# Kernel optimization log

Hardware: AMD Instinct MI355X
Metric: run time of the kernel (lower is better)

The kernel has to match this reference:

```python
import jax, jax.numpy as jnp
import numpy as np

B, C, H, W = 4, 3, 1024, 1024
RADII = (8, 16, 32, 64)
EPS = 1e-5  # BatchNorm2d default eps


def _box_sum(x, r, s):
    # depthwise all-ones conv (kernel r, stride s, VALID padding) == summed box
    return jax.lax.reduce_window(x, 0.0, jax.lax.add, (1, 1, r, r), (1, 1, s, s), 'VALID')


def _axis_interp_ac(x, n_out, axis):
    # bilinear (align_corners=True) interpolation along one axis
    n_in = x.shape[axis]
    pos = jnp.arange(n_out, dtype=x.dtype) * ((n_in - 1) / max(n_out - 1, 1))
    i0 = jnp.clip(jnp.floor(pos).astype(jnp.int32), 0, n_in - 2)
    w = pos - i0.astype(x.dtype)
    a = jnp.take(x, i0, axis=axis)
    b = jnp.take(x, i0 + 1, axis=axis)
    shape = [1] * x.ndim
    shape[axis] = n_out
    w = w.reshape(shape)
    return a * (1 - w) + b * w


def _resize_ac(x, oh, ow):
    x = _axis_interp_ac(x, oh, 2)
    x = _axis_interp_ac(x, ow, 3)
    return x


def _bn(x, g, b, rm, rv):
    inv = g / jnp.sqrt(rv + EPS)
    return x * inv[None, :, None, None] + (b - rm * inv)[None, :, None, None]


def _forward(guide, src, w1, g1, b1, rm1, rv1, w2, g2, b2, rm2, rv2, w3):
    Hg, Wg = guide.shape[2], guide.shape[3]
    gg = guide * guide
    gs = guide * src
    ones = jnp.ones((1, guide.shape[1], Hg, Wg), guide.dtype)
    stats = []
    for r in RADII:
        s = r // 2
        N = _box_sum(ones, r, s)
        mx = _box_sum(guide, r, s) / N
        my = _box_sum(src, r, s) / N
        cov = _box_sum(gs, r, s) / N - mx * my
        var = _box_sum(gg, r, s) / N - mx * mx
        stats.append((mx, my, cov, var))
    mx1, my1, cov1, var1 = stats[0]
    oh, ow = cov1.shape[2], cov1.shape[3]
    feats = [cov1, var1]
    for (_, _, cov, var) in stats[1:]:
        feats.append(_resize_ac(cov, oh, ow))
        feats.append(_resize_ac(var, oh, ow))
    x = jnp.concatenate(feats, axis=1)  # [B,24,oh,ow]
    x = jax.nn.relu(_bn(jnp.einsum('oc,bchw->bohw', w1, x), g1, b1, rm1, rv1))
    x = jax.nn.relu(_bn(jnp.einsum('oc,bchw->bohw', w2, x), g2, b2, rm2, rv2))
    A = jnp.einsum('oc,bchw->bohw', w3, x)  # [B,3,oh,ow]
    bb = my1 - A * mx1
    mean_A = _resize_ac(A, Hg, Wg)
    mean_b = _resize_ac(bb, Hg, Wg)
    return mean_A * guide + mean_b


def setup_inputs() -> dict:
    key = jax.random.key(0)
    ks = jax.random.split(key, 5)
    f32 = jnp.float32
    return {
        'guide': jax.random.normal(ks[0], (B, C, H, W), f32),
        'src': jax.random.normal(ks[1], (B, C, H, W), f32),
        'w1': jax.random.normal(ks[2], (48, 24), f32) * 0.05,
        'g1': jnp.ones((48,), f32), 'b1': jnp.zeros((48,), f32),
        'rm1': jnp.zeros((48,), f32), 'rv1': jnp.ones((48,), f32),
        'w2': jax.random.normal(ks[3], (48, 48), f32) * 0.05,
        'g2': jnp.ones((48,), f32), 'b2': jnp.zeros((48,), f32),
        'rm2': jnp.zeros((48,), f32), 'rv2': jnp.ones((48,), f32),
        'w3': jax.random.normal(ks[4], (3, 48), f32) * 0.05,
    }


def reference(guide, src, w1, g1, b1, rm1, rv1, w2, g2, b2, rm2, rv2, w3):
    return _forward(guide, src, w1, g1, b1, rm1, rv1, w2, g2, b2, rm2, rv2, w3)
```

## Files before the change

### kernel.cpp

```cpp
#include <hip/hip_runtime.h>

#define HH 1024
#define WW 1024
#define NB 4
#define NC 3
#define BC 12
#define N1 255
#define N2 127
#define N3 63
#define N4 31
#define EPS 1e-5f

constexpr size_t S8_OFF  = 0;
constexpr size_t S8_SZ   = 4ull * BC * N1 * N1;
constexpr size_t S16_OFF = S8_OFF + S8_SZ;
constexpr size_t S16_SZ  = 4ull * BC * N2 * N2;
constexpr size_t S32_OFF = S16_OFF + S16_SZ;
constexpr size_t S32_SZ  = 4ull * BC * N3 * N3;
constexpr size_t S64_OFF = S32_OFF + S32_SZ;
constexpr size_t S64_SZ  = 4ull * BC * N4 * N4;
constexpr size_t CV16_OFF = S64_OFF + S64_SZ;
constexpr size_t CV16_SZ  = 2ull * BC * N2 * N2;
constexpr size_t CV32_OFF = CV16_OFF + CV16_SZ;
constexpr size_t CV32_SZ  = 2ull * BC * N3 * N3;
constexpr size_t CV64_OFF = CV32_OFF + CV32_SZ;
constexpr size_t CV64_SZ  = 2ull * BC * N4 * N4;
constexpr size_t A_OFF    = CV64_OFF + CV64_SZ;
constexpr size_t A_SZ     = (size_t)NB * NC * N1 * N1;
constexpr size_t BB_OFF   = A_OFF + A_SZ;

__global__ __launch_bounds__(256) void base_kernel(
    const float* __restrict__ guide, const float* __restrict__ src,
    float* __restrict__ S8)
{
    int blk = blockIdx.x;
    int bc  = blk / N1;
    int i   = blk % N1;
    int j   = threadIdx.x;
    if (j >= N1) return;

    const float* g0 = guide + (size_t)bc * HH * WW + (size_t)(4 * i) * WW + 4 * j;
    const float* s0 = src   + (size_t)bc * HH * WW + (size_t)(4 * i) * WW + 4 * j;

    float sg = 0.f, ss = 0.f, sgg = 0.f, sgs = 0.f;
#pragma unroll
    for (int r = 0; r < 8; ++r) {
        float4 ga = *(const float4*)(g0 + (size_t)r * WW);
        float4 gb = *(const float4*)(g0 + (size_t)r * WW + 4);
        float4 sa = *(const float4*)(s0 + (size_t)r * WW);
        float4 sb = *(const float4*)(s0 + (size_t)r * WW + 4);
        float ge[8] = {ga.x, ga.y, ga.z, ga.w, gb.x, gb.y, gb.z, gb.w};
        float se[8] = {sa.x, sa.y, sa.z, sa.w, sb.x, sb.y, sb.z, sb.w};
#pragma unroll
        for (int k = 0; k < 8; ++k) {
            float g = ge[k], s = se[k];
            sg  += g;
            ss  += s;
            sgg += g * g;
            sgs += g * s;
        }
    }
    size_t qs  = (size_t)BC * N1 * N1;
    size_t idx = (size_t)bc * N1 * N1 + (size_t)i * N1 + j;
    S8[0 * qs + idx] = sg;
    S8[1 * qs + idx] = ss;
    S8[2 * qs + idx] = sgg;
    S8[3 * qs + idx] = sgs;
}

__global__ __launch_bounds__(256) void pyr_kernel(
    const float* __restrict__ Sin, float* __restrict__ Sout,
    float* __restrict__ CVout, int nin, int nout, float invN)
{
    int idx = blockIdx.x * blockDim.x + threadIdx.x;
    int total = BC * nout * nout;
    if (idx >= total) return;
    int j  = idx % nout;
    int t  = idx / nout;
    int i  = t % nout;
    int bc = t / nout;

    size_t sIn  = (size_t)BC * nin * nin;
    size_t base = (size_t)bc * nin * nin;
    int p = 2 * i, q = 2 * j;

    float sums[4];
#pragma unroll
    for (int qt = 0; qt < 4; ++qt) {
        const float* P = Sin + (size_t)qt * sIn + base;
        sums[qt] = P[(size_t)p * nin + q] + P[(size_t)(p + 2) * nin + q] +
                   P[(size_t)p * nin + q + 2] + P[(size_t)(p + 2) * nin + q + 2];
    }
    size_t sOut = (size_t)BC * nout * nout;
    size_t o    = (size_t)bc * nout * nout + (size_t)i * nout + j;
    Sout[0 * sOut + o] = sums[0];
    Sout[1 * sOut + o] = sums[1];
    Sout[2 * sOut + o] = sums[2];
    Sout[3 * sOut + o] = sums[3];
    float mx = sums[0] * invN, my = sums[1] * invN;
    CVout[o]        = sums[3] * invN - mx * my;
    CVout[sOut + o] = sums[2] * invN - mx * mx;
}

__global__ __launch_bounds__(256) void mlp_kernel(
    const float* __restrict__ S8,
    const float* __restrict__ CV16, const float* __restrict__ CV32,
    const float* __restrict__ CV64,
    const float* __restrict__ w1, const float* __restrict__ g1,
    const float* __restrict__ b1, const float* __restrict__ rm1,
    const float* __restrict__ rv1,
    const float* __restrict__ w2, const float* __restrict__ g2,
    const float* __restrict__ b2, const float* __restrict__ rm2,
    const float* __restrict__ rv2,
    const float* __restrict__ w3,
    float* __restrict__ A, float* __restrict__ Bb)
{
    __shared__ float sw1[48 * 24], sw2[48 * 48], sw3[3 * 48];
    __shared__ float inv1[48], bia1[48], inv2[48], bia2[48];
    int t = threadIdx.x;
    for (int k = t; k < 48 * 24; k += 256) sw1[k] = w1[k];
    for (int k = t; k < 48 * 48; k += 256) sw2[k] = w2[k];
    for (int k = t; k < 3 * 48; k += 256) sw3[k] = w3[k];
    if (t < 48) {
        float iv = g1[t] * rsqrtf(rv1[t] + EPS);
        inv1[t] = iv; bia1[t] = b1[t] - rm1[t] * iv;
        float iv2 = g2[t] * rsqrtf(rv2[t] + EPS);
        inv2[t] = iv2; bia2[t] = b2[t] - rm2[t] * iv2;
    }
    __syncthreads();

    int idx = blockIdx.x * 256 + t;
    if (idx >= NB * N1 * N1) return;
    int ox = idx % N1;
    int r  = idx / N1;
    int oy = r % N1;
    int b  = r / N1;

    float feats[24], mx1[3], my1[3];

    size_t s8q = (size_t)BC * N1 * N1;
    for (int c = 0; c < 3; ++c) {
        size_t o = (size_t)(b * 3 + c) * N1 * N1 + (size_t)oy * N1 + ox;
        float sg = S8[o], ss = S8[s8q + o], sgg = S8[2 * s8q + o], sgs = S8[3 * s8q + o];
        float mx = sg * (1.f / 64.f), my = ss * (1.f / 64.f);
        mx1[c] = mx; my1[c] = my;
        feats[c]     = sgs * (1.f / 64.f) - mx * my;
        feats[3 + c] = sgg * (1.f / 64.f) - mx * mx;
    }

    const float* CVs[3] = {CV16, CV32, CV64};
    const int nins[3]   = {N2, N3, N4};
    const float scales[3] = {(float)(126.0 / 254.0), (float)(62.0 / 254.0),
                             (float)(30.0 / 254.0)};
#pragma unroll
    for (int l = 0; l < 3; ++l) {
        const float* CV = CVs[l];
        int nin = nins[l];
        float sc = scales[l];
        float py = (float)oy * sc;
        int   i0 = min(max((int)floorf(py), 0), nin - 2);
        float wy = py - (float)i0;
        float px = (float)ox * sc;
        int   j0 = min(max((int)floorf(px), 0), nin - 2);
        float wx = px - (float)j0;
        size_t cvq = (size_t)BC * nin * nin;
        int fo = 6 + 6 * l;
        for (int c = 0; c < 3; ++c) {
            size_t bix = (size_t)(b * 3 + c) * nin * nin;
            size_t o00 = bix + (size_t)i0 * nin + j0;
            float c00 = CV[o00], c01 = CV[o00 + 1];
            float c10 = CV[o00 + nin], c11 = CV[o00 + nin + 1];
            feats[fo + c] = (c00 * (1.f - wy) + c10 * wy) * (1.f - wx) +
                            (c01 * (1.f - wy) + c11 * wy) * wx;
            float v00 = CV[cvq + o00], v01 = CV[cvq + o00 + 1];
            float v10 = CV[cvq + o00 + nin], v11 = CV[cvq + o00 + nin + 1];
            feats[fo + 3 + c] = (v00 * (1.f - wy) + v10 * wy) * (1.f - wx) +
                                (v01 * (1.f - wy) + v11 * wy) * wx;
        }
    }

    float h1[48];
#pragma unroll
    for (int o = 0; o < 48; ++o) {
        float acc = 0.f;
#pragma unroll
        for (int c = 0; c < 24; ++c) acc += sw1[o * 24 + c] * feats[c];
        h1[o] = fmaxf(acc * inv1[o] + bia1[o], 0.f);
    }
    float h2[48];
#pragma unroll
    for (int o = 0; o < 48; ++o) {
        float acc = 0.f;
#pragma unroll
        for (int c = 0; c < 48; ++c) acc += sw2[o * 48 + c] * h1[c];
        h2[o] = fmaxf(acc * inv2[o] + bia2[o], 0.f);
    }
#pragma unroll
    for (int c = 0; c < 3; ++c) {
        float acc = 0.f;
#pragma unroll
        for (int k = 0; k < 48; ++k) acc += sw3[c * 48 + k] * h2[k];
        size_t o = (size_t)(b * 3 + c) * N1 * N1 + (size_t)oy * N1 + ox;
        A[o]  = acc;
        Bb[o] = my1[c] - acc * mx1[c];
    }
}

__global__ __launch_bounds__(256) void final_kernel(
    const float* __restrict__ guide, const float* __restrict__ A,
    const float* __restrict__ Bb, float* __restrict__ out)
{
    __shared__ float aH[N1 + 1], bH[N1 + 1];
    int blk = blockIdx.x;
    int bc  = blk / HH;
    int h   = blk % HH;

    const float scale = (float)(254.0 / 1023.0);
    float py = (float)h * scale;
    int   i0 = min(max((int)floorf(py), 0), N1 - 2);
    float wy = py - (float)i0;

    int t = threadIdx.x;
    if (t < N1) {
        size_t base = (size_t)bc * N1 * N1 + (size_t)i0 * N1 + t;
        aH[t] = A[base] * (1.f - wy) + A[base + N1] * wy;
        bH[t] = Bb[base] * (1.f - wy) + Bb[base + N1] * wy;
    }
    __syncthreads();

    const float* gp = guide + (size_t)bc * HH * WW + (size_t)h * WW;
    float*       op = out   + (size_t)bc * HH * WW + (size_t)h * WW;

    float4 g4 = *(const float4*)(gp + 4 * t);
    float4 o4;
    float ge[4] = {g4.x, g4.y, g4.z, g4.w};
    float oe[4];
#pragma unroll
    for (int k = 0; k < 4; ++k) {
        int w = 4 * t + k;
        float px = (float)w * scale;
        int   j0 = min(max((int)floorf(px), 0), N1 - 2);
        float wx = px - (float)j0;
        float a = aH[j0] * (1.f - wx) + aH[j0 + 1] * wx;
        float bbv = bH[j0] * (1.f - wx) + bH[j0 + 1] * wx;
        oe[k] = a * ge[k] + bbv;
    }
    o4.x = oe[0]; o4.y = oe[1]; o4.z = oe[2]; o4.w = oe[3];
    *(float4*)(op + 4 * t) = o4;
}

extern "C" void kernel_launch(void* const* d_in, const int* in_sizes, int n_in,
                              void* d_out, int out_size, void* d_ws, size_t ws_size,
                              hipStream_t stream)
{
    const float* guide = (const float*)d_in[0];
    const float* src   = (const float*)d_in[1];
    const float* w1    = (const float*)d_in[2];
    const float* g1    = (const float*)d_in[3];
    const float* b1    = (const float*)d_in[4];
    const float* rm1   = (const float*)d_in[5];
    const float* rv1   = (const float*)d_in[6];
    const float* w2    = (const float*)d_in[7];
    const float* g2    = (const float*)d_in[8];
    const float* b2    = (const float*)d_in[9];
    const float* rm2   = (const float*)d_in[10];
    const float* rv2   = (const float*)d_in[11];
    const float* w3    = (const float*)d_in[12];
    float*       out   = (float*)d_out;

    float* ws   = (float*)d_ws;
    float* S8   = ws + S8_OFF;
    float* S16  = ws + S16_OFF;
    float* S32  = ws + S32_OFF;
    float* S64  = ws + S64_OFF;
    float* CV16 = ws + CV16_OFF;
    float* CV32 = ws + CV32_OFF;
    float* CV64 = ws + CV64_OFF;
    float* Abuf = ws + A_OFF;
    float* Bbuf = ws + BB_OFF;

    base_kernel<<<BC * N1, 256, 0, stream>>>(guide, src, S8);

    {
        int total = BC * N2 * N2;
        pyr_kernel<<<(total + 255) / 256, 256, 0, stream>>>(S8, S16, CV16, N1, N2,
                                                            1.f / 256.f);
    }
    {
        int total = BC * N3 * N3;
        pyr_kernel<<<(total + 255) / 256, 256, 0, stream>>>(S16, S32, CV32, N2, N3,
                                                            1.f / 1024.f);
    }
    {
        int total = BC * N4 * N4;
        pyr_kernel<<<(total + 255) / 256, 256, 0, stream>>>(S32, S64, CV64, N3, N4,
                                                            1.f / 4096.f);
    }

    {
        int total = NB * N1 * N1;
        mlp_kernel<<<(total + 255) / 256, 256, 0, stream>>>(
            S8, CV16, CV32, CV64, w1, g1, b1, rm1, rv1, w2, g2, b2, rm2, rv2, w3,
            Abuf, Bbuf);
    }

    final_kernel<<<BC * HH, 256, 0, stream>>>(guide, Abuf, Bbuf, out);
}
```

Measured before the change: 234.4 us.

## Restructure box-sum pass, fuse pyramid levels, pack MLP math into float2

The base kernel now has each block read 12 input rows once. It forms the overlapping 8-row vertical sums from 4-row partials and does the horizontal reduction through shared memory. Before, each 8x8 window re-read its overlapping rows and columns. The three pyramid launches become one kernel that builds every level straight from S8, which drops the intermediate S16/S32/S64 buffers but makes coarse levels do more reads. The MLP kernel moves to 128-thread blocks and uses two-wide float vectors so packed FMA can be used.

```diff
diff --git a/kernel.cpp b/kernel.cpp
--- a/kernel.cpp
+++ b/kernel.cpp
@@ -1,4 +1,6 @@
 #include <hip/hip_runtime.h>
+
+typedef float v2f __attribute__((ext_vector_type(2)));
 
 #define HH 1024
 #define WW 1024
@@ -13,13 +15,7 @@
 
 constexpr size_t S8_OFF  = 0;
 constexpr size_t S8_SZ   = 4ull * BC * N1 * N1;
-constexpr size_t S16_OFF = S8_OFF + S8_SZ;
-constexpr size_t S16_SZ  = 4ull * BC * N2 * N2;
-constexpr size_t S32_OFF = S16_OFF + S16_SZ;
-constexpr size_t S32_SZ  = 4ull * BC * N3 * N3;
-constexpr size_t S64_OFF = S32_OFF + S32_SZ;
-constexpr size_t S64_SZ  = 4ull * BC * N4 * N4;
-constexpr size_t CV16_OFF = S64_OFF + S64_SZ;
+constexpr size_t CV16_OFF = S8_OFF + S8_SZ;
 constexpr size_t CV16_SZ  = 2ull * BC * N2 * N2;
 constexpr size_t CV32_OFF = CV16_OFF + CV16_SZ;
 constexpr size_t CV32_SZ  = 2ull * BC * N3 * N3;
@@ -33,76 +29,122 @@
     const float* __restrict__ guide, const float* __restrict__ src,
     float* __restrict__ S8)
 {
-    int blk = blockIdx.x;
-    int bc  = blk / N1;
-    int i   = blk % N1;
-    int j   = threadIdx.x;
-    if (j >= N1) return;
-
-    const float* g0 = guide + (size_t)bc * HH * WW + (size_t)(4 * i) * WW + 4 * j;
-    const float* s0 = src   + (size_t)bc * HH * WW + (size_t)(4 * i) * WW + 4 * j;
-
-    float sg = 0.f, ss = 0.f, sgg = 0.f, sgs = 0.f;
-#pragma unroll
-    for (int r = 0; r < 8; ++r) {
-        float4 ga = *(const float4*)(g0 + (size_t)r * WW);
-        float4 gb = *(const float4*)(g0 + (size_t)r * WW + 4);
-        float4 sa = *(const float4*)(s0 + (size_t)r * WW);
-        float4 sb = *(const float4*)(s0 + (size_t)r * WW + 4);
-        float ge[8] = {ga.x, ga.y, ga.z, ga.w, gb.x, gb.y, gb.z, gb.w};
-        float se[8] = {sa.x, sa.y, sa.z, sa.w, sb.x, sb.y, sb.z, sb.w};
-#pragma unroll
-        for (int k = 0; k < 8; ++k) {
-            float g = ge[k], s = se[k];
-            sg  += g;
-            ss  += s;
-            sgg += g * g;
-            sgs += g * s;
-        }
-    }
-    size_t qs  = (size_t)BC * N1 * N1;
-    size_t idx = (size_t)bc * N1 * N1 + (size_t)i * N1 + j;
-    S8[0 * qs + idx] = sg;
-    S8[1 * qs + idx] = ss;
-    S8[2 * qs + idx] = sgg;
-    S8[3 * qs + idx] = sgs;
-}
-
-__global__ __launch_bounds__(256) void pyr_kernel(
-    const float* __restrict__ Sin, float* __restrict__ Sout,
-    float* __restrict__ CVout, int nin, int nout, float invN)
-{
-    int idx = blockIdx.x * blockDim.x + threadIdx.x;
-    int total = BC * nout * nout;
-    if (idx >= total) return;
-    int j  = idx % nout;
-    int t  = idx / nout;
-    int i  = t % nout;
-    int bc = t / nout;
-
-    size_t sIn  = (size_t)BC * nin * nin;
-    size_t base = (size_t)bc * nin * nin;
-    int p = 2 * i, q = 2 * j;
-
-    float sums[4];
-#pragma unroll
-    for (int qt = 0; qt < 4; ++qt) {
-        const float* P = Sin + (size_t)qt * sIn + base;
-        sums[qt] = P[(size_t)p * nin + q] + P[(size_t)(p + 2) * nin + q] +
-                   P[(size_t)p * nin + q + 2] + P[(size_t)(p + 2) * nin + q + 2];
-    }
+    __shared__ float smem[8][WW];
+
+    int b  = blockIdx.x % 128;
+    int bc = blockIdx.x / 128;
+    int t  = threadIdx.x;
+
+    const float* gbase = guide + (size_t)bc * HH * WW + 4 * t;
+    const float* sbase = src   + (size_t)bc * HH * WW + 4 * t;
+
+    float pg[3][4], ps[3][4], pgg[3][4], pgs[3][4];
+#pragma unroll
+    for (int grp = 0; grp < 3; ++grp)
+#pragma unroll
+        for (int k = 0; k < 4; ++k) {
+            pg[grp][k] = 0.f; ps[grp][k] = 0.f;
+            pgg[grp][k] = 0.f; pgs[grp][k] = 0.f;
+        }
+
+#pragma unroll
+    for (int grp = 0; grp < 3; ++grp) {
+#pragma unroll
+        for (int r = 0; r < 4; ++r) {
+            int row = 8 * b + 4 * grp + r;
+            if (row < HH) {
+                float4 g4 = *(const float4*)(gbase + (size_t)row * WW);
+                float4 s4 = *(const float4*)(sbase + (size_t)row * WW);
+                float ge[4] = {g4.x, g4.y, g4.z, g4.w};
+                float se[4] = {s4.x, s4.y, s4.z, s4.w};
+#pragma unroll
+                for (int k = 0; k < 4; ++k) {
+                    pg[grp][k]  += ge[k];
+                    ps[grp][k]  += se[k];
+                    pgg[grp][k] += ge[k] * ge[k];
+                    pgs[grp][k] += ge[k] * se[k];
+                }
+            }
+        }
+    }
+
+#pragma unroll
+    for (int k = 0; k < 4; ++k) {
+        int c = 4 * t + k;
+        smem[0][c] = pg[0][k]  + pg[1][k];
+        smem[1][c] = ps[0][k]  + ps[1][k];
+        smem[2][c] = pgg[0][k] + pgg[1][k];
+        smem[3][c] = pgs[0][k] + pgs[1][k];
+        smem[4][c] = pg[1][k]  + pg[2][k];
+        smem[5][c] = ps[1][k]  + ps[2][k];
+        smem[6][c] = pgg[1][k] + pgg[2][k];
+        smem[7][c] = pgs[1][k] + pgs[2][k];
+    }
+    __syncthreads();
+
+    if (t < N1) {
+        size_t qs   = (size_t)BC * N1 * N1;
+        size_t base = (size_t)bc * N1 * N1;
+#pragma unroll
+        for (int rsel = 0; rsel < 2; ++rsel) {
+            int i = 2 * b + rsel;
+            if (i < N1) {
+#pragma unroll
+                for (int q = 0; q < 4; ++q) {
+                    const float* arr = smem[4 * rsel + q];
+                    float4 a4 = *(const float4*)(arr + 4 * t);
+                    float4 b4 = *(const float4*)(arr + 4 * t + 4);
+                    float v = (a4.x + a4.y) + (a4.z + a4.w) +
+                              (b4.x + b4.y) + (b4.z + b4.w);
+                    S8[(size_t)q * qs + base + (size_t)i * N1 + t] = v;
+                }
+            }
+        }
+    }
+}
+
+__global__ __launch_bounds__(256) void pyr_all(
+    const float* __restrict__ S8, float* __restrict__ CV16,
+    float* __restrict__ CV32, float* __restrict__ CV64)
+{
+    const int n2t = BC * N2 * N2, n3t = BC * N3 * N3, n4t = BC * N4 * N4;
+    int idx = blockIdx.x * 256 + threadIdx.x;
+
+    float* CV; int nout, cnt; float invN; int rem;
+    if (idx < n2t)              { CV = CV16; nout = N2; cnt = 2; invN = 1.f / 256.f;  rem = idx; }
+    else if (idx < n2t + n3t)   { CV = CV32; nout = N3; cnt = 4; invN = 1.f / 1024.f; rem = idx - n2t; }
+    else if (idx < n2t + n3t + n4t) { CV = CV64; nout = N4; cnt = 8; invN = 1.f / 4096.f; rem = idx - n2t - n3t; }
+    else return;
+
+    int j  = rem % nout;
+    int tt = rem / nout;
+    int i  = tt % nout;
+    int bc = tt / nout;
+
+    size_t qs = (size_t)BC * N1 * N1;
+    const float* P = S8 + (size_t)bc * N1 * N1;
+    int p0 = cnt * i, q0 = cnt * j;
+
+    float s0 = 0.f, s1 = 0.f, s2 = 0.f, s3 = 0.f;
+    for (int ky = 0; ky < cnt; ++ky) {
+        size_t roff = (size_t)(p0 + 2 * ky) * N1 + q0;
+        for (int kx = 0; kx < cnt; ++kx) {
+            size_t o = roff + 2 * kx;
+            s0 += P[0 * qs + o];
+            s1 += P[1 * qs + o];
+            s2 += P[2 * qs + o];
+            s3 += P[3 * qs + o];
+        }
+    }
+
     size_t sOut = (size_t)BC * nout * nout;
     size_t o    = (size_t)bc * nout * nout + (size_t)i * nout + j;
-    Sout[0 * sOut + o] = sums[0];
-    Sout[1 * sOut + o] = sums[1];
-    Sout[2 * sOut + o] = sums[2];
-    Sout[3 * sOut + o] = sums[3];
-    float mx = sums[0] * invN, my = sums[1] * invN;
-    CVout[o]        = sums[3] * invN - mx * my;
-    CVout[sOut + o] = sums[2] * invN - mx * mx;
-}
-
-__global__ __launch_bounds__(256) void mlp_kernel(
+    float mx = s0 * invN, my = s1 * invN;
+    CV[o]        = s3 * invN - mx * my;
+    CV[sOut + o] = s2 * invN - mx * mx;
+}
+
+__global__ __launch_bounds__(128) void mlp_kernel(
     const float* __restrict__ S8,
     const float* __restrict__ CV16, const float* __restrict__ CV32,
     const float* __restrict__ CV64,
@@ -118,9 +160,9 @@
     __shared__ float sw1[48 * 24], sw2[48 * 48], sw3[3 * 48];
     __shared__ float inv1[48], bia1[48], inv2[48], bia2[48];
     int t = threadIdx.x;
-    for (int k = t; k < 48 * 24; k += 256) sw1[k] = w1[k];
-    for (int k = t; k < 48 * 48; k += 256) sw2[k] = w2[k];
-    for (int k = t; k < 3 * 48; k += 256) sw3[k] = w3[k];
+    for (int k = t; k < 48 * 24; k += 128) sw1[k] = w1[k];
+    for (int k = t; k < 48 * 48; k += 128) sw2[k] = w2[k];
+    for (int k = t; k < 3 * 48; k += 128) sw3[k] = w3[k];
     if (t < 48) {
         float iv = g1[t] * rsqrtf(rv1[t] + EPS);
         inv1[t] = iv; bia1[t] = b1[t] - rm1[t] * iv;
@@ -129,7 +171,7 @@
     }
     __syncthreads();
 
-    int idx = blockIdx.x * 256 + t;
+    int idx = blockIdx.x * 128 + t;
     if (idx >= NB * N1 * N1) return;
     int ox = idx % N1;
     int r  = idx / N1;
@@ -139,6 +181,7 @@
     float feats[24], mx1[3], my1[3];
 
     size_t s8q = (size_t)BC * N1 * N1;
+#pragma unroll
     for (int c = 0; c < 3; ++c) {
         size_t o = (size_t)(b * 3 + c) * N1 * N1 + (size_t)oy * N1 + ox;
         float sg = S8[o], ss = S8[s8q + o], sgg = S8[2 * s8q + o], sgs = S8[3 * s8q + o];
@@ -165,6 +208,7 @@
         float wx = px - (float)j0;
         size_t cvq = (size_t)BC * nin * nin;
         int fo = 6 + 6 * l;
+#pragma unroll
         for (int c = 0; c < 3; ++c) {
             size_t bix = (size_t)(b * 3 + c) * nin * nin;
             size_t o00 = bix + (size_t)i0 * nin + j0;
@@ -179,30 +223,40 @@
         }
     }
 
-    float h1[48];
+    v2f f2[12];
+#pragma unroll
+    for (int k = 0; k < 12; ++k) { f2[k][0] = feats[2 * k]; f2[k][1] = feats[2 * k + 1]; }
+
+    v2f h1v[24];
 #pragma unroll
     for (int o = 0; o < 48; ++o) {
-        float acc = 0.f;
-#pragma unroll
-        for (int c = 0; c < 24; ++c) acc += sw1[o * 24 + c] * feats[c];
-        h1[o] = fmaxf(acc * inv1[o] + bia1[o], 0.f);
-    }
-    float h2[48];
+        const v2f* wrow = (const v2f*)(&sw1[o * 24]);
+        v2f acc = {0.f, 0.f};
+#pragma unroll
+        for (int c = 0; c < 12; ++c) acc += wrow[c] * f2[c];
+        float v = fmaxf((acc[0] + acc[1]) * inv1[o] + bia1[o], 0.f);
+        h1v[o >> 1][o & 1] = v;
+    }
+    v2f h2v[24];
 #pragma unroll
     for (int o = 0; o < 48; ++o) {
-        float acc = 0.f;
-#pragma unroll
-        for (int c = 0; c < 48; ++c) acc += sw2[o * 48 + c] * h1[c];
-        h2[o] = fmaxf(acc * inv2[o] + bia2[o], 0.f);
+        const v2f* wrow = (const v2f*)(&sw2[o * 48]);
+        v2f acc = {0.f, 0.f};
+#pragma unroll
+        for (int c = 0; c < 24; ++c) acc += wrow[c] * h1v[c];
+        float v = fmaxf((acc[0] + acc[1]) * inv2[o] + bia2[o], 0.f);
+        h2v[o >> 1][o & 1] = v;
     }
 #pragma unroll
     for (int c = 0; c < 3; ++c) {
-        float acc = 0.f;
-#pragma unroll
-        for (int k = 0; k < 48; ++k) acc += sw3[c * 48 + k] * h2[k];
+        const v2f* wrow = (const v2f*)(&sw3[c * 48]);
+        v2f acc = {0.f, 0.f};
+#pragma unroll
+        for (int k = 0; k < 24; ++k) acc += wrow[k] * h2v[k];
+        float a = acc[0] + acc[1];
         size_t o = (size_t)(b * 3 + c) * N1 * N1 + (size_t)oy * N1 + ox;
-        A[o]  = acc;
-        Bb[o] = my1[c] - acc * mx1[c];
+        A[o]  = a;
+        Bb[o] = my1[c] - a * mx1[c];
     }
 }
 
@@ -232,7 +286,6 @@
     float*       op = out   + (size_t)bc * HH * WW + (size_t)h * WW;
 
     float4 g4 = *(const float4*)(gp + 4 * t);
-    float4 o4;
     float ge[4] = {g4.x, g4.y, g4.z, g4.w};
     float oe[4];
 #pragma unroll
@@ -241,11 +294,11 @@
         float px = (float)w * scale;
         int   j0 = min(max((int)floorf(px), 0), N1 - 2);
         float wx = px - (float)j0;
-        float a = aH[j0] * (1.f - wx) + aH[j0 + 1] * wx;
+        float a   = aH[j0] * (1.f - wx) + aH[j0 + 1] * wx;
         float bbv = bH[j0] * (1.f - wx) + bH[j0 + 1] * wx;
         oe[k] = a * ge[k] + bbv;
     }
-    o4.x = oe[0]; o4.y = oe[1]; o4.z = oe[2]; o4.w = oe[3];
+    float4 o4; o4.x = oe[0]; o4.y = oe[1]; o4.z = oe[2]; o4.w = oe[3];
     *(float4*)(op + 4 * t) = o4;
 }
 
@@ -270,36 +323,22 @@
 
     float* ws   = (float*)d_ws;
     float* S8   = ws + S8_OFF;
-    float* S16  = ws + S16_OFF;
-    float* S32  = ws + S32_OFF;
-    float* S64  = ws + S64_OFF;
     float* CV16 = ws + CV16_OFF;
     float* CV32 = ws + CV32_OFF;
     float* CV64 = ws + CV64_OFF;
     float* Abuf = ws + A_OFF;
     float* Bbuf = ws + BB_OFF;
 
-    base_kernel<<<BC * N1, 256, 0, stream>>>(guide, src, S8);
+    base_kernel<<<BC * 128, 256, 0, stream>>>(guide, src, S8);
 
     {
-        int total = BC * N2 * N2;
-        pyr_kernel<<<(total + 255) / 256, 256, 0, stream>>>(S8, S16, CV16, N1, N2,
-                                                            1.f / 256.f);
-    }
-    {
-        int total = BC * N3 * N3;
-        pyr_kernel<<<(total + 255) / 256, 256, 0, stream>>>(S16, S32, CV32, N2, N3,
-                                                            1.f / 1024.f);
-    }
-    {
-        int total = BC * N4 * N4;
-        pyr_kernel<<<(total + 255) / 256, 256, 0, stream>>>(S32, S64, CV64, N3, N4,
-                                                            1.f / 4096.f);
+        int total = BC * (N2 * N2 + N3 * N3 + N4 * N4);
+        pyr_all<<<(total + 255) / 256, 256, 0, stream>>>(S8, CV16, CV32, CV64);
     }
 
     {
         int total = NB * N1 * N1;
-        mlp_kernel<<<(total + 255) / 256, 256, 0, stream>>>(
+        mlp_kernel<<<(total + 127) / 128, 128, 0, stream>>>(
             S8, CV16, CV32, CV64, w1, g1, b1, rm1, rv1, w2, g2, b2, rm2, rv2, w3,
             Abuf, Bbuf);
     }
```

Result: slower. 255.4 us (+8.9%).
